# Kernel tuning notes

Measured on AMD Instinct MI355X. Metric: run time of the kernel, lower is better.

The kernel has to match this reference:

```python
import jax, jax.numpy as jnp
import numpy as np

NUM_HEADS = 8
DIM_HEAD = 32
WINDOW = 8
SHIFT = 4
C = NUM_HEADS * DIM_HEAD  # 256


def _relative_position_index(w):
    coords = np.stack(np.meshgrid(np.arange(w), np.arange(w), indexing='ij'))  # [2,w,w]
    cf = coords.reshape(2, -1)                       # [2, w*w]
    rel = cf[:, :, None] - cf[:, None, :]            # [2, N, N]
    rel = rel.transpose(1, 2, 0) + (w - 1)           # [N, N, 2]
    rel = rel * np.array([2 * w - 1, 1])
    return rel.sum(-1)                               # [N, N] int

REL_IDX = jnp.asarray(_relative_position_index(WINDOW))  # [64,64]


def setup_inputs() -> dict:
    key = jax.random.key(0)
    ks = jax.random.split(key, 4)
    B, H, W = 4, 256, 256
    x = jax.random.normal(ks[0], (B, H, W, C), dtype=jnp.float32)
    w_qkv = jax.random.normal(ks[1], (C, 3 * C), dtype=jnp.float32) * 0.02
    b_qkv = jnp.zeros((3 * C,), dtype=jnp.float32)
    w_proj = jax.random.normal(ks[2], (C, C), dtype=jnp.float32) * 0.02
    b_proj = jnp.zeros((C,), dtype=jnp.float32)
    bias_table = jax.random.normal(ks[3], ((2 * WINDOW - 1) ** 2, NUM_HEADS), dtype=jnp.float32) * 0.02
    return {"x": x, "w_qkv": w_qkv, "b_qkv": b_qkv, "w_proj": w_proj, "b_proj": b_proj, "bias_table": bias_table}


def _window_partition(x, w):
    B, H, W_, Ch = x.shape
    x = x.reshape(B, H // w, w, W_ // w, w, Ch)
    x = x.transpose(0, 1, 3, 2, 4, 5)
    return x.reshape(-1, w, w, Ch)


def _window_reverse(windows, w, H, W_):
    Ch = windows.shape[-1]
    x = windows.reshape(-1, H // w, W_ // w, w, w, Ch)
    x = x.transpose(0, 1, 3, 2, 4, 5)
    return x.reshape(-1, H, W_, Ch)


def reference(x, w_qkv, b_qkv, w_proj, b_proj, bias_table):
    B, H, W_, Ch = x.shape
    N = WINDOW * WINDOW
    shifted = jnp.roll(x, (-SHIFT, -SHIFT), axis=(1, 2)) if SHIFT > 0 else x
    xw = _window_partition(shifted, WINDOW).reshape(-1, N, Ch)   # [nWB, 64, C]
    qkv = xw @ w_qkv + b_qkv                                      # [nWB, 64, 3C]
    qkv = qkv.reshape(-1, N, 3, NUM_HEADS, DIM_HEAD).transpose(2, 0, 3, 1, 4)
    q, k, v = qkv[0], qkv[1], qkv[2]                              # [nWB, h, 64, d]
    q = q * (DIM_HEAD ** -0.5)
    attn = jnp.einsum('whnd,whmd->whnm', q, k)                    # [nWB, h, 64, 64]
    rel_bias = bias_table[REL_IDX.reshape(-1)].reshape(N, N, NUM_HEADS).transpose(2, 0, 1)
    attn = jax.nn.softmax(attn + rel_bias, axis=-1)
    out = jnp.einsum('whnm,whmd->whnd', attn, v)                  # [nWB, h, 64, d]
    out = out.transpose(0, 2, 1, 3).reshape(-1, WINDOW, WINDOW, Ch)
    shifted_out = _window_reverse(out, WINDOW, H, W_)
    y = jnp.roll(shifted_out, (SHIFT, SHIFT), axis=(1, 2)) if SHIFT > 0 else shifted_out
    return y @ w_proj + b_proj
```

## Files before the change

### kernel.cpp

```cpp
#include <hip/hip_runtime.h>
#include <hip/hip_bf16.h>

typedef __attribute__((ext_vector_type(8))) short bf16x8;
typedef __attribute__((ext_vector_type(4))) float f32x4;
typedef __attribute__((ext_vector_type(2))) __bf16 bf16x2t;

#define MFMA(a, b, c) __builtin_amdgcn_mfma_f32_16x16x32_bf16(a, b, c, 0, 0, 0)

__device__ __forceinline__ unsigned int pack2(float x, float y) {
  bf16x2t v;
  v.x = (__bf16)x; v.y = (__bf16)y;
  union { bf16x2t v; unsigned u; } c;
  c.v = v;
  return c.u;
}
__device__ __forceinline__ unsigned short f2bf(float x) {
  union { float f; unsigned u; } a{x};
  unsigned r = a.u + 0x7FFFu + ((a.u >> 16) & 1u);
  return (unsigned short)(r >> 16);
}
__device__ __forceinline__ bf16x8 pack8(f32x4 a, f32x4 b) {
  union { unsigned u[4]; bf16x8 v; } r;
  r.u[0] = pack2(a[0], a[1]); r.u[1] = pack2(a[2], a[3]);
  r.u[2] = pack2(b[0], b[1]); r.u[3] = pack2(b[2], b[3]);
  return r.v;
}

__device__ __forceinline__ int src_off(int t) {
  int wi = t >> 6, n = t & 63;
  int b = wi >> 10, wr = (wi >> 5) & 31, wc = wi & 31;
  int hh = (wr * 8 + (n >> 3) + 4) & 255;
  int ww = (wc * 8 + (n & 7) + 4) & 255;
  return ((((b << 8) | hh) << 8) | ww) << 8;
}

__global__ __launch_bounds__(256) void prep_kernel(
    const float* __restrict__ w_qkv, const float* __restrict__ w_proj,
    const float* __restrict__ bias_table,
    unsigned short* __restrict__ wqkvt, unsigned short* __restrict__ wpt,
    float* __restrict__ rb2) {
  int i = blockIdx.x * 256 + threadIdx.x;
  if (i < 196608) {
    wqkvt[i] = f2bf(w_qkv[(i & 255) * 768 + (i >> 8)]);
  } else if (i < 262144) {
    int j = i - 196608;
    wpt[j] = f2bf(w_proj[(j & 255) * 256 + (j >> 8)]);
  } else {
    int j = i - 262144;
    int jr = j & 3, ln = (j >> 2) & 15, g = (j >> 6) & 3;
    int nt = (j >> 8) & 3, mt = (j >> 10) & 3, h = j >> 12;
    int q = 16 * nt + ln;
    int k = 16 * mt + 4 * g + jr;
    int idx = ((q >> 3) - (k >> 3) + 7) * 15 + ((q & 7) - (k & 7) + 7);
    rb2[j] = bias_table[idx * 8 + h];
  }
}

__global__ __launch_bounds__(512, 4) void fused_kernel(
    const float* __restrict__ x, const unsigned short* __restrict__ wqkvt,
    const float* __restrict__ b_qkv, const unsigned short* __restrict__ wpt,
    const float* __restrict__ b_proj, const float* __restrict__ rb2,
    float* __restrict__ y) {
  __shared__ unsigned short sm[36864];
  int wi = blockIdx.x;
  int tid = threadIdx.x;
  int h = tid >> 6, lane = tid & 63, ln = lane & 15, g = lane >> 4;
  unsigned short* R1 = sm + 16384 + h * 2560;

  int tb = wi * 64;
  {
    int tok0 = tid >> 4, ck = tid & 15;
    int tok1 = tok0 + 32;
    const float4* s0 = (const float4*)(x + src_off(tb + tok0) + ck * 16);
    const float4* s1 = (const float4*)(x + src_off(tb + tok1) + ck * 16);
    float4 a0 = s0[0], a1 = s0[1], a2 = s0[2], a3 = s0[3];
    float4 b0 = s1[0], b1 = s1[1], b2 = s1[2], b3 = s1[3];
    uint4 w0, w1;
    w0.x = pack2(a0.x, a0.y); w0.y = pack2(a0.z, a0.w);
    w0.z = pack2(a1.x, a1.y); w0.w = pack2(a1.z, a1.w);
    w1.x = pack2(a2.x, a2.y); w1.y = pack2(a2.z, a2.w);
    w1.z = pack2(a3.x, a3.y); w1.w = pack2(a3.z, a3.w);
    int base0 = tok0 * 512 + ck * 32, swz0 = (tok0 & 7) << 4;
    *(uint4*)((char*)sm + ((base0) ^ swz0)) = w0;
    *(uint4*)((char*)sm + ((base0 + 16) ^ swz0)) = w1;
    w0.x = pack2(b0.x, b0.y); w0.y = pack2(b0.z, b0.w);
    w0.z = pack2(b1.x, b1.y); w0.w = pack2(b1.z, b1.w);
    w1.x = pack2(b2.x, b2.y); w1.y = pack2(b2.z, b2.w);
    w1.z = pack2(b3.x, b3.y); w1.w = pack2(b3.z, b3.w);
    int base1 = tok1 * 512 + ck * 32, swz1 = (tok1 & 7) << 4;
    *(uint4*)((char*)sm + ((base1) ^ swz1)) = w0;
    *(uint4*)((char*)sm + ((base1 + 16) ^ swz1)) = w1;
  }
  __syncthreads();

  {
    f32x4 av[4][2] = {};
#pragma unroll 2
    for (int ks = 0; ks < 8; ++ks) {
      bf16x8 xf[4];
#pragma unroll
      for (int t = 0; t < 4; ++t) {
        int row = 16 * t + ln;
        xf[t] = *(const bf16x8*)((char*)sm + ((row * 512 + ks * 64 + 16 * g) ^ ((row & 7) << 4)));
      }
      bf16x8 wv[2];
#pragma unroll
      for (int dt = 0; dt < 2; ++dt)
        wv[dt] = *(const bf16x8*)(wqkvt + (512 + 32 * h + 16 * dt + ln) * 256 + ks * 32 + 8 * g);
      __builtin_amdgcn_s_setprio(1);
#pragma unroll
      for (int mt = 0; mt < 4; ++mt)
#pragma unroll
        for (int dt = 0; dt < 2; ++dt)
          av[mt][dt] = MFMA(xf[mt], wv[dt], av[mt][dt]);
      __builtin_amdgcn_s_setprio(0);
    }
#pragma unroll
    for (int dt = 0; dt < 2; ++dt) {
      float bv_ = b_qkv[512 + 32 * h + 16 * dt + ln];
#pragma unroll
      for (int mt = 0; mt < 4; ++mt) {
        uint2 vp;
        vp.x = pack2(av[mt][dt][0] + bv_, av[mt][dt][1] + bv_);
        vp.y = pack2(av[mt][dt][2] + bv_, av[mt][dt][3] + bv_);
        *(uint2*)&R1[(16 * dt + ln) * 72 + 32 * (mt >> 1) + 8 * g + 4 * (mt & 1)] = vp;
      }
    }
  }

  bf16x8 qf[4], kf[4];
  {
    f32x4 accq[2][4] = {}, acck[2][4] = {};
#pragma unroll 1
    for (int ks = 0; ks < 8; ++ks) {
      bf16x8 xf[4];
#pragma unroll
      for (int t = 0; t < 4; ++t) {
        int row = 16 * t + ln;
        xf[t] = *(const bf16x8*)((char*)sm + ((row * 512 + ks * 64 + 16 * g) ^ ((row & 7) << 4)));
      }
      bf16x8 wq[2], wk[2];
#pragma unroll
      for (int mt = 0; mt < 2; ++mt) {
        int nr = 32 * h + 16 * mt + ln;
        wq[mt] = *(const bf16x8*)(wqkvt + nr * 256 + ks * 32 + 8 * g);
        wk[mt] = *(const bf16x8*)(wqkvt + (256 + nr) * 256 + ks * 32 + 8 * g);
      }
      __builtin_amdgcn_s_setprio(1);
#pragma unroll
      for (int mt = 0; mt < 2; ++mt)
#pragma unroll
        for (int nt = 0; nt < 4; ++nt) {
          accq[mt][nt] = MFMA(wq[mt], xf[nt], accq[mt][nt]);
          acck[mt][nt] = MFMA(wk[mt], xf[nt], acck[mt][nt]);
        }
      __builtin_amdgcn_s_setprio(0);
    }
    f32x4 bq0 = *(const f32x4*)(b_qkv + 32 * h + 4 * g);
    f32x4 bq1 = *(const f32x4*)(b_qkv + 32 * h + 16 + 4 * g);
    f32x4 bk0 = *(const f32x4*)(b_qkv + 256 + 32 * h + 4 * g);
    f32x4 bk1 = *(const f32x4*)(b_qkv + 256 + 32 * h + 16 + 4 * g);
    const float sc = 0.17677669529663687f;
#pragma unroll
    for (int nt = 0; nt < 4; ++nt) {
      qf[nt] = pack8((accq[0][nt] + bq0) * sc, (accq[1][nt] + bq1) * sc);
      kf[nt] = pack8(acck[0][nt] + bk0, acck[1][nt] + bk1);
    }
  }

  f32x4 st[4][4];
  const float* rbw = rb2 + h * 4096;
#pragma unroll
  for (int mt = 0; mt < 4; ++mt)
#pragma unroll
    for (int nt = 0; nt < 4; ++nt)
      st[mt][nt] = *(const f32x4*)(rbw + ((((mt * 4 + nt) * 4 + g) * 16 + ln) * 4));
  __builtin_amdgcn_s_setprio(1);
#pragma unroll
  for (int mt = 0; mt < 4; ++mt)
#pragma unroll
    for (int nt = 0; nt < 4; ++nt)
      st[mt][nt] = MFMA(kf[mt], qf[nt], st[mt][nt]);
  __builtin_amdgcn_s_setprio(0);

  bf16x8 vf[2][2];
#pragma unroll
  for (int kk = 0; kk < 2; ++kk)
#pragma unroll
    for (int nd = 0; nd < 2; ++nd)
      vf[kk][nd] = *(const bf16x8*)&R1[(16 * nd + ln) * 72 + 32 * kk + 8 * g];

  bf16x8 pb[2][4];
#pragma unroll
  for (int nt = 0; nt < 4; ++nt) {
    f32x4 ma, mb;
#pragma unroll
    for (int jr = 0; jr < 4; ++jr) {
      ma[jr] = fmaxf(st[0][nt][jr], st[1][nt][jr]);
      mb[jr] = fmaxf(st[2][nt][jr], st[3][nt][jr]);
    }
    float mx = fmaxf(fmaxf(fmaxf(ma[0], mb[0]), fmaxf(ma[1], mb[1])),
                     fmaxf(fmaxf(ma[2], mb[2]), fmaxf(ma[3], mb[3])));
    mx = fmaxf(mx, __shfl_xor(mx, 16));
    mx = fmaxf(mx, __shfl_xor(mx, 32));
    f32x4 e0, e1, e2, e3;
#pragma unroll
    for (int jr = 0; jr < 4; ++jr) {
      e0[jr] = __expf(st[0][nt][jr] - mx);
      e1[jr] = __expf(st[1][nt][jr] - mx);
      e2[jr] = __expf(st[2][nt][jr] - mx);
      e3[jr] = __expf(st[3][nt][jr] - mx);
    }
    f32x4 s01 = e0 + e1, s23 = e2 + e3;
    float sum = (s01[0] + s23[0]) + (s01[1] + s23[1])
              + ((s01[2] + s23[2]) + (s01[3] + s23[3]));
    sum += __shfl_xor(sum, 16);
    sum += __shfl_xor(sum, 32);
    float inv = 1.f / sum;
    pb[0][nt] = pack8(e0 * inv, e1 * inv);
    pb[1][nt] = pack8(e2 * inv, e3 * inv);
  }

  f32x4 o[2][4] = {};
  __builtin_amdgcn_s_setprio(1);
#pragma unroll
  for (int kk = 0; kk < 2; ++kk)
#pragma unroll
    for (int dt = 0; dt < 2; ++dt)
#pragma unroll
      for (int nt = 0; nt < 4; ++nt)
        o[dt][nt] = MFMA(vf[kk][dt], pb[kk][nt], o[dt][nt]);
  __builtin_amdgcn_s_setprio(0);

#pragma unroll
  for (int dt = 0; dt < 2; ++dt)
#pragma unroll
    for (int nt = 0; nt < 4; ++nt) {
      uint2 vp;
      vp.x = pack2(o[dt][nt][0], o[dt][nt][1]);
      vp.y = pack2(o[dt][nt][2], o[dt][nt][3]);
      *(uint2*)&R1[(16 * nt + ln) * 40 + 16 * dt + 4 * g] = vp;
    }
  __syncthreads();

  f32x4 a2[4][2] = {};
#pragma unroll 2
  for (int ks = 0; ks < 8; ++ks) {
    const unsigned short* AO = sm + 16384 + ks * 2560;
    bf16x8 af2[4], bf2[2];
#pragma unroll
    for (int mt = 0; mt < 4; ++mt)
      af2[mt] = *(const bf16x8*)&AO[(16 * mt + ln) * 40 + 8 * g];
#pragma unroll
    for (int nt = 0; nt < 2; ++nt)
      bf2[nt] = *(const bf16x8*)(wpt + (32 * h + 16 * nt + ln) * 256 + ks * 32 + 8 * g);
    __builtin_amdgcn_s_setprio(1);
#pragma unroll
    for (int mt = 0; mt < 4; ++mt) {
      a2[mt][0] = MFMA(af2[mt], bf2[0], a2[mt][0]);
      a2[mt][1] = MFMA(af2[mt], bf2[1], a2[mt][1]);
    }
    __builtin_amdgcn_s_setprio(0);
  }
  int b = wi >> 10, wr = (wi >> 5) & 31, wc = wi & 31;
  int hb = wr * 8 + (g >> 1) + 4;
  int wb = wc * 8 + 4 * (g & 1) + 4;
  int colb = 32 * h + ln;
  float bp0 = b_proj[colb], bp1 = b_proj[colb + 16];
#pragma unroll
  for (int mt = 0; mt < 4; ++mt) {
    int hh = (hb + 2 * mt) & 255;
#pragma unroll
    for (int jr = 0; jr < 4; ++jr) {
      int ww = (wb + jr) & 255;
      float* yp = y + (((((b << 8) | hh) << 8) | ww) << 8) + colb;
      yp[0]  = a2[mt][0][jr] + bp0;
      yp[16] = a2[mt][1][jr] + bp1;
    }
  }
}

extern "C" void kernel_launch(void* const* d_in, const int* in_sizes, int n_in,
                              void* d_out, int out_size, void* d_ws, size_t ws_size,
                              hipStream_t stream) {
  const float* x          = (const float*)d_in[0];
  const float* w_qkv      = (const float*)d_in[1];
  const float* b_qkv      = (const float*)d_in[2];
  const float* w_proj     = (const float*)d_in[3];
  const float* b_proj     = (const float*)d_in[4];
  const float* bias_table = (const float*)d_in[5];
  char* ws = (char*)d_ws;
  unsigned short* wqkvt = (unsigned short*)(ws);
  unsigned short* wpt   = (unsigned short*)(ws + 393216);
  float* rb2            = (float*)(ws + 524288);
  float* y = (float*)d_out;

  prep_kernel<<<1152, 256, 0, stream>>>(w_qkv, w_proj, bias_table, wqkvt, wpt, rb2);
  fused_kernel<<<4096, 512, 0, stream>>>(x, wqkvt, b_qkv, wpt, b_proj, rb2, y);
}
```

Baseline: 337.9 us.

## Shrink LDS and registers to raise occupancy by splitting QKV and softmax phases

V is now kept in registers instead of LDS, and the attention output overwrites the X tile region, with a barrier added before the overwrite. This cuts shared memory from 72KB to 32KB. Q and K projections run in separate loops, and the score/softmax/PV stage processes query columns in two halves, both to lower peak register pressure. Launch bounds are raised to 6 waves-per-EU-equivalent blocks and the setprio hints are removed, trading some X-tile LDS re-reads and an extra barrier for more resident blocks.

Result: slower. 523.0 us (+54.8%).

```diff
diff --git a/kernel.cpp b/kernel.cpp
--- a/kernel.cpp
+++ b/kernel.cpp
@@ -56,16 +56,16 @@
   }
 }
 
-__global__ __launch_bounds__(512, 4) void fused_kernel(
+__global__ __launch_bounds__(512, 6) void fused_kernel(
     const float* __restrict__ x, const unsigned short* __restrict__ wqkvt,
     const float* __restrict__ b_qkv, const unsigned short* __restrict__ wpt,
     const float* __restrict__ b_proj, const float* __restrict__ rb2,
     float* __restrict__ y) {
-  __shared__ unsigned short sm[36864];
+  __shared__ unsigned short sm[16384];
   int wi = blockIdx.x;
   int tid = threadIdx.x;
   int h = tid >> 6, lane = tid & 63, ln = lane & 15, g = lane >> 4;
-  unsigned short* R1 = sm + 16384 + h * 2560;
+  int swl = (ln & 7) << 4;
 
   int tb = wi * 64;
   {
@@ -93,8 +93,67 @@
   }
   __syncthreads();
 
+  bf16x8 qf[4];
   {
-    f32x4 av[4][2] = {};
+    f32x4 accq[2][4] = {};
+#pragma unroll 1
+    for (int ks = 0; ks < 8; ++ks) {
+      bf16x8 xf[4];
+#pragma unroll
+      for (int t = 0; t < 4; ++t) {
+        int row = 16 * t + ln;
+        xf[t] = *(const bf16x8*)((char*)sm + ((row * 512 + ks * 64 + 16 * g) ^ ((row & 7) << 4)));
+      }
+      bf16x8 wq[2];
+#pragma unroll
+      for (int mt = 0; mt < 2; ++mt)
+        wq[mt] = *(const bf16x8*)(wqkvt + (32 * h + 16 * mt + ln) * 256 + ks * 32 + 8 * g);
+#pragma unroll
+      for (int mt = 0; mt < 2; ++mt)
+#pragma unroll
+        for (int nt = 0; nt < 4; ++nt)
+          accq[mt][nt] = MFMA(wq[mt], xf[nt], accq[mt][nt]);
+    }
+    const float sc = 0.17677669529663687f;
+    f32x4 bq0 = *(const f32x4*)(b_qkv + 32 * h + 4 * g) * sc;
+    f32x4 bq1 = *(const f32x4*)(b_qkv + 32 * h + 16 + 4 * g) * sc;
+#pragma unroll
+    for (int nt = 0; nt < 4; ++nt)
+      qf[nt] = pack8(accq[0][nt] * sc + bq0, accq[1][nt] * sc + bq1);
+  }
+
+  bf16x8 kf[4];
+  {
+    f32x4 acck[2][4] = {};
+#pragma unroll 1
+    for (int ks = 0; ks < 8; ++ks) {
+      bf16x8 xf[4];
+#pragma unroll
+      for (int t = 0; t < 4; ++t) {
+        int row = 16 * t + ln;
+        xf[t] = *(const bf16x8*)((char*)sm + ((row * 512 + ks * 64 + 16 * g) ^ ((row & 7) << 4)));
+      }
+      bf16x8 wk[2];
+#pragma unroll
+      for (int mt = 0; mt < 2; ++mt)
+        wk[mt] = *(const bf16x8*)(wqkvt + (256 + 32 * h + 16 * mt + ln) * 256 + ks * 32 + 8 * g);
+#pragma unroll
+      for (int mt = 0; mt < 2; ++mt)
+#pragma unroll
+        for (int nt = 0; nt < 4; ++nt)
+          acck[mt][nt] = MFMA(wk[mt], xf[nt], acck[mt][nt]);
+    }
+    f32x4 bk0 = *(const f32x4*)(b_qkv + 256 + 32 * h + 4 * g);
+    f32x4 bk1 = *(const f32x4*)(b_qkv + 256 + 32 * h + 16 + 4 * g);
+#pragma unroll
+    for (int nt = 0; nt < 4; ++nt)
+      kf[nt] = pack8(acck[0][nt] + bk0, acck[1][nt] + bk1);
+  }
+
+  bf16x8 vf[2][2];
+#pragma unroll
+  for (int dt = 0; dt < 2; ++dt) {
+    f32x4 av[4] = {};
 #pragma unroll 2
     for (int ks = 0; ks < 8; ++ks) {
       bf16x8 xf[4];
@@ -103,164 +162,104 @@
         int row = 16 * t + ln;
         xf[t] = *(const bf16x8*)((char*)sm + ((row * 512 + ks * 64 + 16 * g) ^ ((row & 7) << 4)));
       }
-      bf16x8 wv[2];
+      bf16x8 wv = *(const bf16x8*)(wqkvt + (512 + 32 * h + 16 * dt + ln) * 256 + ks * 32 + 8 * g);
+#pragma unroll
+      for (int mt = 0; mt < 4; ++mt)
+        av[mt] = MFMA(xf[mt], wv, av[mt]);
+    }
+    float bv = b_qkv[512 + 32 * h + 16 * dt + ln];
+    f32x4 bvv = {bv, bv, bv, bv};
+    vf[0][dt] = pack8(av[0] + bvv, av[1] + bvv);
+    vf[1][dt] = pack8(av[2] + bvv, av[3] + bvv);
+  }
+  __syncthreads();
+
+  char* OVL = (char*)sm + h * 4096;
+  const float* rbw = rb2 + h * 4096;
+
+#pragma unroll
+  for (int H = 0; H < 2; ++H) {
+    f32x4 st[4][2];
+#pragma unroll
+    for (int mt = 0; mt < 4; ++mt)
+#pragma unroll
+      for (int n = 0; n < 2; ++n)
+        st[mt][n] = *(const f32x4*)(rbw + ((((mt * 4 + (2 * H + n)) * 4 + g) * 16 + ln) * 4));
+#pragma unroll
+    for (int mt = 0; mt < 4; ++mt)
+#pragma unroll
+      for (int n = 0; n < 2; ++n)
+        st[mt][n] = MFMA(kf[mt], qf[2 * H + n], st[mt][n]);
+
+    bf16x8 pb[2][2];
+#pragma unroll
+    for (int n = 0; n < 2; ++n) {
+      f32x4 ma, mb;
+#pragma unroll
+      for (int jr = 0; jr < 4; ++jr) {
+        ma[jr] = fmaxf(st[0][n][jr], st[1][n][jr]);
+        mb[jr] = fmaxf(st[2][n][jr], st[3][n][jr]);
+      }
+      float mx = fmaxf(fmaxf(fmaxf(ma[0], mb[0]), fmaxf(ma[1], mb[1])),
+                       fmaxf(fmaxf(ma[2], mb[2]), fmaxf(ma[3], mb[3])));
+      mx = fmaxf(mx, __shfl_xor(mx, 16));
+      mx = fmaxf(mx, __shfl_xor(mx, 32));
+      f32x4 e0, e1, e2, e3;
+#pragma unroll
+      for (int jr = 0; jr < 4; ++jr) {
+        e0[jr] = __expf(st[0][n][jr] - mx);
+        e1[jr] = __expf(st[1][n][jr] - mx);
+        e2[jr] = __expf(st[2][n][jr] - mx);
+        e3[jr] = __expf(st[3][n][jr] - mx);
+      }
+      f32x4 s01 = e0 + e1, s23 = e2 + e3;
+      float sum = (s01[0] + s23[0]) + (s01[1] + s23[1])
+                + ((s01[2] + s23[2]) + (s01[3] + s23[3]));
+      sum += __shfl_xor(sum, 16);
+      sum += __shfl_xor(sum, 32);
+      float inv = 1.f / sum;
+      pb[0][n] = pack8(e0 * inv, e1 * inv);
+      pb[1][n] = pack8(e2 * inv, e3 * inv);
+    }
+
+    f32x4 o[2][2] = {};
+#pragma unroll
+    for (int kk = 0; kk < 2; ++kk)
 #pragma unroll
       for (int dt = 0; dt < 2; ++dt)
-        wv[dt] = *(const bf16x8*)(wqkvt + (512 + 32 * h + 16 * dt + ln) * 256 + ks * 32 + 8 * g);
-      __builtin_amdgcn_s_setprio(1);
-#pragma unroll
-      for (int mt = 0; mt < 4; ++mt)
-#pragma unroll
-        for (int dt = 0; dt < 2; ++dt)
-          av[mt][dt] = MFMA(xf[mt], wv[dt], av[mt][dt]);
-      __builtin_amdgcn_s_setprio(0);
-    }
-#pragma unroll
-    for (int dt = 0; dt < 2; ++dt) {
-      float bv_ = b_qkv[512 + 32 * h + 16 * dt + ln];
-#pragma unroll
-      for (int mt = 0; mt < 4; ++mt) {
+#pragma unroll
+        for (int n = 0; n < 2; ++n)
+          o[dt][n] = MFMA(vf[kk][dt], pb[kk][n], o[dt][n]);
+
+#pragma unroll
+    for (int dt = 0; dt < 2; ++dt)
+#pragma unroll
+      for (int n = 0; n < 2; ++n) {
         uint2 vp;
-        vp.x = pack2(av[mt][dt][0] + bv_, av[mt][dt][1] + bv_);
-        vp.y = pack2(av[mt][dt][2] + bv_, av[mt][dt][3] + bv_);
-        *(uint2*)&R1[(16 * dt + ln) * 72 + 32 * (mt >> 1) + 8 * g + 4 * (mt & 1)] = vp;
-      }
-    }
-  }
-
-  bf16x8 qf[4], kf[4];
-  {
-    f32x4 accq[2][4] = {}, acck[2][4] = {};
-#pragma unroll 1
-    for (int ks = 0; ks < 8; ++ks) {
-      bf16x8 xf[4];
-#pragma unroll
-      for (int t = 0; t < 4; ++t) {
-        int row = 16 * t + ln;
-        xf[t] = *(const bf16x8*)((char*)sm + ((row * 512 + ks * 64 + 16 * g) ^ ((row & 7) << 4)));
-      }
-      bf16x8 wq[2], wk[2];
-#pragma unroll
-      for (int mt = 0; mt < 2; ++mt) {
-        int nr = 32 * h + 16 * mt + ln;
-        wq[mt] = *(const bf16x8*)(wqkvt + nr * 256 + ks * 32 + 8 * g);
-        wk[mt] = *(const bf16x8*)(wqkvt + (256 + nr) * 256 + ks * 32 + 8 * g);
-      }
-      __builtin_amdgcn_s_setprio(1);
-#pragma unroll
-      for (int mt = 0; mt < 2; ++mt)
-#pragma unroll
-        for (int nt = 0; nt < 4; ++nt) {
-          accq[mt][nt] = MFMA(wq[mt], xf[nt], accq[mt][nt]);
-          acck[mt][nt] = MFMA(wk[mt], xf[nt], acck[mt][nt]);
-        }
-      __builtin_amdgcn_s_setprio(0);
-    }
-    f32x4 bq0 = *(const f32x4*)(b_qkv + 32 * h + 4 * g);
-    f32x4 bq1 = *(const f32x4*)(b_qkv + 32 * h + 16 + 4 * g);
-    f32x4 bk0 = *(const f32x4*)(b_qkv + 256 + 32 * h + 4 * g);
-    f32x4 bk1 = *(const f32x4*)(b_qkv + 256 + 32 * h + 16 + 4 * g);
-    const float sc = 0.17677669529663687f;
-#pragma unroll
-    for (int nt = 0; nt < 4; ++nt) {
-      qf[nt] = pack8((accq[0][nt] + bq0) * sc, (accq[1][nt] + bq1) * sc);
-      kf[nt] = pack8(acck[0][nt] + bk0, acck[1][nt] + bk1);
-    }
-  }
-
-  f32x4 st[4][4];
-  const float* rbw = rb2 + h * 4096;
-#pragma unroll
-  for (int mt = 0; mt < 4; ++mt)
-#pragma unroll
-    for (int nt = 0; nt < 4; ++nt)
-      st[mt][nt] = *(const f32x4*)(rbw + ((((mt * 4 + nt) * 4 + g) * 16 + ln) * 4));
-  __builtin_amdgcn_s_setprio(1);
-#pragma unroll
-  for (int mt = 0; mt < 4; ++mt)
-#pragma unroll
-    for (int nt = 0; nt < 4; ++nt)
-      st[mt][nt] = MFMA(kf[mt], qf[nt], st[mt][nt]);
-  __builtin_amdgcn_s_setprio(0);
-
-  bf16x8 vf[2][2];
-#pragma unroll
-  for (int kk = 0; kk < 2; ++kk)
-#pragma unroll
-    for (int nd = 0; nd < 2; ++nd)
-      vf[kk][nd] = *(const bf16x8*)&R1[(16 * nd + ln) * 72 + 32 * kk + 8 * g];
-
-  bf16x8 pb[2][4];
-#pragma unroll
-  for (int nt = 0; nt < 4; ++nt) {
-    f32x4 ma, mb;
-#pragma unroll
-    for (int jr = 0; jr < 4; ++jr) {
-      ma[jr] = fmaxf(st[0][nt][jr], st[1][nt][jr]);
-      mb[jr] = fmaxf(st[2][nt][jr], st[3][nt][jr]);
-    }
-    float mx = fmaxf(fmaxf(fmaxf(ma[0], mb[0]), fmaxf(ma[1], mb[1])),
-                     fmaxf(fmaxf(ma[2], mb[2]), fmaxf(ma[3], mb[3])));
-    mx = fmaxf(mx, __shfl_xor(mx, 16));
-    mx = fmaxf(mx, __shfl_xor(mx, 32));
-    f32x4 e0, e1, e2, e3;
-#pragma unroll
-    for (int jr = 0; jr < 4; ++jr) {
-      e0[jr] = __expf(st[0][nt][jr] - mx);
-      e1[jr] = __expf(st[1][nt][jr] - mx);
-      e2[jr] = __expf(st[2][nt][jr] - mx);
-      e3[jr] = __expf(st[3][nt][jr] - mx);
-    }
-    f32x4 s01 = e0 + e1, s23 = e2 + e3;
-    float sum = (s01[0] + s23[0]) + (s01[1] + s23[1])
-              + ((s01[2] + s23[2]) + (s01[3] + s23[3]));
-    sum += __shfl_xor(sum, 16);
-    sum += __shfl_xor(sum, 32);
-    float inv = 1.f / sum;
-    pb[0][nt] = pack8(e0 * inv, e1 * inv);
-    pb[1][nt] = pack8(e2 * inv, e3 * inv);
-  }
-
-  f32x4 o[2][4] = {};
-  __builtin_amdgcn_s_setprio(1);
-#pragma unroll
-  for (int kk = 0; kk < 2; ++kk)
-#pragma unroll
-    for (int dt = 0; dt < 2; ++dt)
-#pragma unroll
-      for (int nt = 0; nt < 4; ++nt)
-        o[dt][nt] = MFMA(vf[kk][dt], pb[kk][nt], o[dt][nt]);
-  __builtin_amdgcn_s_setprio(0);
-
-#pragma unroll
-  for (int dt = 0; dt < 2; ++dt)
-#pragma unroll
-    for (int nt = 0; nt < 4; ++nt) {
-      uint2 vp;
-      vp.x = pack2(o[dt][nt][0], o[dt][nt][1]);
-      vp.y = pack2(o[dt][nt][2], o[dt][nt][3]);
-      *(uint2*)&R1[(16 * nt + ln) * 40 + 16 * dt + 4 * g] = vp;
-    }
+        vp.x = pack2(o[dt][n][0], o[dt][n][1]);
+        vp.y = pack2(o[dt][n][2], o[dt][n][3]);
+        int byte = ((16 * (2 * H + n) + ln) * 64 + 32 * dt + 8 * g) ^ swl;
+        *(uint2*)(OVL + byte) = vp;
+      }
+  }
   __syncthreads();
 
   f32x4 a2[4][2] = {};
 #pragma unroll 2
   for (int ks = 0; ks < 8; ++ks) {
-    const unsigned short* AO = sm + 16384 + ks * 2560;
+    const char* AO = (const char*)sm + ks * 4096;
     bf16x8 af2[4], bf2[2];
 #pragma unroll
     for (int mt = 0; mt < 4; ++mt)
-      af2[mt] = *(const bf16x8*)&AO[(16 * mt + ln) * 40 + 8 * g];
+      af2[mt] = *(const bf16x8*)(AO + (((16 * mt + ln) * 64 + 16 * g) ^ swl));
 #pragma unroll
     for (int nt = 0; nt < 2; ++nt)
       bf2[nt] = *(const bf16x8*)(wpt + (32 * h + 16 * nt + ln) * 256 + ks * 32 + 8 * g);
-    __builtin_amdgcn_s_setprio(1);
 #pragma unroll
     for (int mt = 0; mt < 4; ++mt) {
       a2[mt][0] = MFMA(af2[mt], bf2[0], a2[mt][0]);
       a2[mt][1] = MFMA(af2[mt], bf2[1], a2[mt][1]);
     }
-    __builtin_amdgcn_s_setprio(0);
   }
   int b = wi >> 10, wr = (wi >> 5) & 31, wc = wi & 31;
   int hb = wr * 8 + (g >> 1) + 4;
```
